# Kernel tuning notes

Hardware: AMD Instinct MI355X
Metric: run time of the kernel (lower is better)

The kernel has to match this reference:

```python
import jax, jax.numpy as jnp
import numpy as np

N = 100000      # nodes
E = 1250000     # edges
F_IN = 32       # node_feat_dim
H = 64          # hidden_dim (hard-coded in module)
R = 8           # num_relations
G = 256         # graphs in batch
EMB = 16        # embedding_dim
OUT = 1         # output_dim
EPS = 1e-5


def setup_inputs() -> dict:
    key = jax.random.key(0)
    ks = jax.random.split(key, 40)
    w = lambda k, shape: (jax.random.normal(k, shape, jnp.float32) * 0.05)
    inp = {
        'x': jax.random.normal(ks[0], (N, F_IN), jnp.float32),
        'edge_index': jax.random.randint(ks[1], (2, E), 0, N),
        'edge_type': jax.random.randint(ks[2], (E,), 0, R),
        'batch': jnp.sort(jax.random.randint(ks[3], (N,), 0, G)),
        # RGCN layer params: per-relation weight, root weight, bias
        'conv1_w': w(ks[4], (R, F_IN, H)), 'conv1_root': w(ks[5], (F_IN, H)), 'conv1_b': jnp.zeros((H,), jnp.float32),
        'bn1_g': jnp.ones((H,), jnp.float32), 'bn1_b': jnp.zeros((H,), jnp.float32),
        'conv2_w': w(ks[6], (R, H, H)), 'conv2_root': w(ks[7], (H, H)), 'conv2_b': jnp.zeros((H,), jnp.float32),
        'bn2_g': jnp.ones((H,), jnp.float32), 'bn2_b': jnp.zeros((H,), jnp.float32),
        'conv3_w': w(ks[8], (R, H, H)), 'conv3_root': w(ks[9], (H, H)), 'conv3_b': jnp.zeros((H,), jnp.float32),
        'bn3_g': jnp.ones((H,), jnp.float32), 'bn3_b': jnp.zeros((H,), jnp.float32),
        # fc_emb: Linear(384->128), BN(128), LeakyReLU, Dropout(eval=id), Linear(128->EMB)
        'fc1_w': w(ks[10], (3 * H * 2, 128)), 'fc1_b': jnp.zeros((128,), jnp.float32),
        'fcbn_g': jnp.ones((128,), jnp.float32), 'fcbn_b': jnp.zeros((128,), jnp.float32),
        'fc2_w': w(ks[11], (128, EMB)), 'fc2_b': jnp.zeros((EMB,), jnp.float32),
        # decoder: Linear(EMB->64), LeakyReLU, Linear(64->OUT)
        'dec1_w': w(ks[12], (EMB, 64)), 'dec1_b': jnp.zeros((64,), jnp.float32),
        'dec2_w': w(ks[13], (64, OUT)), 'dec2_b': jnp.zeros((OUT,), jnp.float32),
    }
    return inp


def _leaky(z):
    return jnp.where(z > 0, z, 0.2 * z)


def _bn(x, g, b):  # training-mode batch norm, biased variance
    mu = x.mean(axis=0)
    var = x.var(axis=0)
    return g * (x - mu) * jax.lax.rsqrt(var + EPS) + b


def _rgcn(x, W, root, bias, src, dst, edge_type):
    # out_i = x_i @ root + bias + sum_r mean_{j in N_r(i)} x_j @ W_r
    out = x @ root + bias
    for r in range(R):
        mask = (edge_type == r).astype(x.dtype)           # [E]
        h = x @ W[r]                                      # [N, out]
        msg = h[src] * mask[:, None]                      # gather + mask
        s = jax.ops.segment_sum(msg, dst, num_segments=N)  # scatter-add
        cnt = jax.ops.segment_sum(mask, dst, num_segments=N)
        out = out + s / jnp.maximum(cnt, 1.0)[:, None]
    return out


def reference(x, edge_index, edge_type, batch,
              conv1_w, conv1_root, conv1_b, bn1_g, bn1_b,
              conv2_w, conv2_root, conv2_b, bn2_g, bn2_b,
              conv3_w, conv3_root, conv3_b, bn3_g, bn3_b,
              fc1_w, fc1_b, fcbn_g, fcbn_b, fc2_w, fc2_b,
              dec1_w, dec1_b, dec2_w, dec2_b):
    src, dst = edge_index[0], edge_index[1]
    x1 = jax.nn.relu(_bn(_rgcn(x, conv1_w, conv1_root, conv1_b, src, dst, edge_type), bn1_g, bn1_b))
    x2 = jax.nn.relu(_bn(_rgcn(x1, conv2_w, conv2_root, conv2_b, src, dst, edge_type), bn2_g, bn2_b))
    x3 = jax.nn.relu(_bn(_rgcn(x2, conv3_w, conv3_root, conv3_b, src, dst, edge_type), bn3_g, bn3_b))
    x_all = jnp.concatenate([x1, x2, x3], axis=1)         # [N, 3H]
    ones = jnp.ones((N,), x.dtype)
    cnt = jax.ops.segment_sum(ones, batch, num_segments=G)
    pool_mean = jax.ops.segment_sum(x_all, batch, num_segments=G) / jnp.maximum(cnt, 1.0)[:, None]
    pool_max = jax.ops.segment_max(x_all, batch, num_segments=G)
    pool_max = jnp.where(jnp.isfinite(pool_max), pool_max, 0.0)
    x_graph = jnp.concatenate([pool_mean, pool_max], axis=1)  # [G, 6H]
    h = _leaky(_bn(x_graph @ fc1_w + fc1_b, fcbn_g, fcbn_b))  # dropout = identity (eval)
    emb = h @ fc2_w + fc2_b                                   # [G, EMB]
    pred = _leaky(emb @ dec1_w + dec1_b) @ dec2_w + dec2_b    # [G, OUT]
    return (pred, emb)
```

## Files before the change

### kernel.cpp

```cpp
#include <hip/hip_runtime.h>

#define NN 100000
#define NE 1250000
#define FIN 32
#define HD 64
#define NR 8
#define NG 256
#define BN_EPS 1e-5f
#define PCH 100
#define M_KEYS (NN * NR)
#define NB 782
#define RREP 32
#define HW 576

#if defined(__has_builtin)
#if __has_builtin(__builtin_amdgcn_fdot2_f32_bf16)
#define USE_DOT2 1
#endif
#endif
#ifndef USE_DOT2
#define USE_DOT2 0
#endif

typedef unsigned short ushort_t;
typedef __attribute__((ext_vector_type(8))) short short8;
typedef __attribute__((ext_vector_type(4))) float f32x4;
typedef __attribute__((ext_vector_type(4))) unsigned int u32x4;
#if USE_DOT2
typedef __bf16 bf16x2 __attribute__((ext_vector_type(2)));
#endif

static __device__ __forceinline__ ushort_t f2bf(float f) {
  unsigned u = __float_as_uint(f);
  u += 0x7fffu + ((u >> 16) & 1u);
  return (ushort_t)(u >> 16);
}
static __device__ __forceinline__ float bf2f(ushort_t b) {
  return __uint_as_float((unsigned)b << 16);
}

__global__ void k_zero(float* __restrict__ p, int n) {
  int i = blockIdx.x * 256 + threadIdx.x;
  if (i < n) p[i] = 0.0f;
}

__global__ void k_cnt(const int* __restrict__ dst, const int* __restrict__ ty,
                      unsigned* __restrict__ cnt, int* __restrict__ rank) {
  int e = blockIdx.x * 256 + threadIdx.x;
  if (e < NE) {
    int key = dst[e] * NR + ty[e];
    rank[e] = (int)atomicAdd(&cnt[key], 1u);
  }
}

__global__ void k_scanA(const unsigned* __restrict__ cnt, unsigned* __restrict__ bsum) {
  __shared__ unsigned red[256];
  int t = threadIdx.x;
  int base = blockIdx.x * 1024 + t * 4;
  unsigned s = 0;
  #pragma unroll
  for (int i = 0; i < 4; i++) {
    int idx = base + i;
    if (idx < M_KEYS) s += cnt[idx];
  }
  red[t] = s;
  __syncthreads();
  for (int off = 128; off > 0; off >>= 1) {
    if (t < off) red[t] += red[t + off];
    __syncthreads();
  }
  if (t == 0) bsum[blockIdx.x] = red[0];
}

__global__ __launch_bounds__(1024) void k_scanB(const unsigned* __restrict__ bsum,
                                                unsigned* __restrict__ boff,
                                                int* __restrict__ rowstart) {
  __shared__ unsigned sb[1024];
  int t = threadIdx.x;
  unsigned mine = (t < NB) ? bsum[t] : 0u;
  sb[t] = mine;
  __syncthreads();
  for (int off = 1; off < 1024; off <<= 1) {
    unsigned v = (t >= off) ? sb[t - off] : 0u;
    __syncthreads();
    sb[t] += v;
    __syncthreads();
  }
  if (t < NB) boff[t] = sb[t] - mine;
  if (t == 1023) rowstart[M_KEYS] = (int)sb[1023];
}

__global__ void k_scanC(const unsigned* __restrict__ cnt, const unsigned* __restrict__ boff,
                        int* __restrict__ rowstart) {
  __shared__ unsigned sb[256];
  int t = threadIdx.x;
  int base = blockIdx.x * 1024 + t * 4;
  unsigned c0 = (base + 0 < M_KEYS) ? cnt[base + 0] : 0u;
  unsigned c1 = (base + 1 < M_KEYS) ? cnt[base + 1] : 0u;
  unsigned c2 = (base + 2 < M_KEYS) ? cnt[base + 2] : 0u;
  unsigned c3 = (base + 3 < M_KEYS) ? cnt[base + 3] : 0u;
  unsigned tot = c0 + c1 + c2 + c3;
  sb[t] = tot;
  __syncthreads();
  for (int off = 1; off < 256; off <<= 1) {
    unsigned v = (t >= off) ? sb[t - off] : 0u;
    __syncthreads();
    sb[t] += v;
    __syncthreads();
  }
  unsigned run = boff[blockIdx.x] + (sb[t] - tot);
  if (base + 0 < M_KEYS) rowstart[base + 0] = (int)run; run += c0;
  if (base + 1 < M_KEYS) rowstart[base + 1] = (int)run; run += c1;
  if (base + 2 < M_KEYS) rowstart[base + 2] = (int)run; run += c2;
  if (base + 3 < M_KEYS) rowstart[base + 3] = (int)run;
}

__global__ void k_place(const int* __restrict__ src, const int* __restrict__ dst,
                        const int* __restrict__ ty, const int* __restrict__ rank,
                        const int* __restrict__ rowstart, unsigned* __restrict__ eb) {
  int e = blockIdx.x * 256 + threadIdx.x;
  if (e < NE) {
    int t = ty[e];
    int key = dst[e] * NR + t;
    unsigned off = (unsigned)(src[e] * HW + t * 64);
    eb[rowstart[key] + rank[e]] = (off << 3) | (unsigned)t;
  }
}

template <int F>
__global__ void k_wconv(const float* __restrict__ convw, const float* __restrict__ root,
                        ushort_t* __restrict__ wt) {
  int i = blockIdx.x * 256 + threadIdx.x;
  if (i >= 576 * F) return;
  int c = i / F, k = i % F;
  float v = (c < 512) ? convw[((size_t)(c >> 6) * F + k) * 64 + (c & 63)]
                      : root[(size_t)k * 64 + (c & 63)];
  wt[(size_t)c * F + k] = f2bf(v);
}

template <int F, bool APPLY_BN>
__global__ __launch_bounds__(256) void k_xmm(
    const float* __restrict__ xin, const float* __restrict__ scsh,
    const ushort_t* __restrict__ wt, ushort_t* __restrict__ h) {
  constexpr int KK = 2 * F;
  constexpr int XPAD = KK + 8;
  constexpr int LDR = 592;
  __shared__ ushort_t xs[16 * XPAD];
  __shared__ ushort_t ot[16 * LDR];
  int lane = threadIdx.x & 63;
  int w = threadIdx.x >> 6;
  int m = lane & 15;
  int q = lane >> 4;
  int ct0 = w * 9;

  short8 bfrag[9 * (F / 32)];
  #pragma unroll
  for (int ks = 0; ks < F / 32; ks++)
    #pragma unroll
    for (int t = 0; t < 9; t++)
      bfrag[ks * 9 + t] =
          *(const short8*)(wt + (size_t)((ct0 + t) * 16 + m) * F + ks * 32 + q * 8);

  for (int tile = blockIdx.x; tile < NN / 16; tile += gridDim.x) {
    int nbase = tile * 16;
    for (int i = threadIdx.x; i < 16 * F; i += 256) {
      int r = i / F, k = i - r * F;
      float v = xin[(size_t)(nbase + r) * F + k];
      if (APPLY_BN) v = fmaxf(fmaf(v, scsh[k], scsh[64 + k]), 0.0f);
      ushort_t hi = f2bf(v);
      xs[r * XPAD + k] = hi;
      xs[r * XPAD + F + k] = f2bf(v - bf2f(hi));
    }
    __syncthreads();

    short8 afrag[2 * (F / 32)];
    #pragma unroll
    for (int ks = 0; ks < F / 32; ks++) {
      afrag[2 * ks + 0] = *(const short8*)&xs[m * XPAD + ks * 32 + q * 8];
      afrag[2 * ks + 1] = *(const short8*)&xs[m * XPAD + F + ks * 32 + q * 8];
    }

    f32x4 acc[9];
    #pragma unroll
    for (int t = 0; t < 9; t++) acc[t] = (f32x4){0.f, 0.f, 0.f, 0.f};
    #pragma unroll
    for (int ks = 0; ks < F / 32; ks++) {
      #pragma unroll
      for (int t = 0; t < 9; t++) {
        acc[t] = __builtin_amdgcn_mfma_f32_16x16x32_bf16(afrag[2 * ks + 0],
                                                         bfrag[ks * 9 + t], acc[t], 0, 0, 0);
        acc[t] = __builtin_amdgcn_mfma_f32_16x16x32_bf16(afrag[2 * ks + 1],
                                                         bfrag[ks * 9 + t], acc[t], 0, 0, 0);
      }
    }
    #pragma unroll
    for (int t = 0; t < 9; t++) {
      int col = (ct0 + t) * 16 + m;
      #pragma unroll
      for (int j = 0; j < 4; j++) {
        int row = q * 4 + j;
        ot[row * LDR + col] = f2bf(acc[t][j]);
      }
    }
    __syncthreads();
    u32x4* dst = (u32x4*)(h + (size_t)nbase * HW);
    for (int idx = threadIdx.x; idx < 16 * 72; idx += 256) {
      int row = idx / 72, i = idx - row * 72;
      dst[row * 72 + i] = *(const u32x4*)&ot[row * LDR + i * 8];
    }
  }
}

__global__ __launch_bounds__(256) void k_agg4(
    const ushort_t* __restrict__ h, const int* __restrict__ rs,
    const unsigned* __restrict__ eb, const float* __restrict__ bias,
    float* __restrict__ outp, float* __restrict__ statsrep) {
  __shared__ float red[512];
  __shared__ ushort_t iclu[4][8];
  int lane = threadIdx.x & 63, w = threadIdx.x >> 6;
  int n = blockIdx.x * 4 + w;
  if (lane < 8) {
    int c = rs[n * NR + lane + 1] - rs[n * NR + lane];
    iclu[w][lane] = f2bf(1.0f / (float)(c > 1 ? c : 1));
  }
  int lo = rs[n * NR];
  int cnt = rs[n * NR + NR] - lo;
  __syncthreads();
  int g = lane >> 3;
  int c8 = (lane & 7) * 8;
  float a[8];
  #pragma unroll
  for (int j = 0; j < 8; j++) a[j] = 0.f;
  for (int base = 0; base < cnt; base += 32) {
    unsigned rec[4]; u32x4 hv[4]; unsigned icb[4];
    #pragma unroll
    for (int s = 0; s < 4; s++) {
      int el = base + s * 8 + g;
      rec[s] = eb[lo + (el < cnt ? el : cnt - 1)];
      icb[s] = (el < cnt) ? (unsigned)iclu[w][rec[s] & 7] : 0u;
    }
    #pragma unroll
    for (int s = 0; s < 4; s++)
      hv[s] = *(const u32x4*)(h + (size_t)(rec[s] >> 3) + c8);
#if USE_DOT2
    #pragma unroll
    for (int s = 0; s < 4; s += 2) {
      unsigned b01 = __builtin_amdgcn_perm(icb[s + 1], icb[s], 0x05040100u);
      bf16x2 bb = __builtin_bit_cast(bf16x2, b01);
      #pragma unroll
      for (int k = 0; k < 4; k++) {
        unsigned plo = __builtin_amdgcn_perm(hv[s + 1][k], hv[s][k], 0x05040100u);
        unsigned phi = __builtin_amdgcn_perm(hv[s + 1][k], hv[s][k], 0x07060302u);
        a[2 * k + 0] = __builtin_amdgcn_fdot2_f32_bf16(
            __builtin_bit_cast(bf16x2, plo), bb, a[2 * k + 0], false);
        a[2 * k + 1] = __builtin_amdgcn_fdot2_f32_bf16(
            __builtin_bit_cast(bf16x2, phi), bb, a[2 * k + 1], false);
      }
    }
#else
    #pragma unroll
    for (int s = 0; s < 4; s++) {
      float ic = bf2f((ushort_t)icb[s]);
      #pragma unroll
      for (int k = 0; k < 4; k++) {
        a[2 * k + 0] = fmaf(__uint_as_float(hv[s][k] << 16), ic, a[2 * k + 0]);
        a[2 * k + 1] = fmaf(__uint_as_float(hv[s][k] & 0xffff0000u), ic, a[2 * k + 1]);
      }
    }
#endif
  }
  #pragma unroll
  for (int j = 0; j < 8; j++) {
    a[j] += __shfl_xor(a[j], 8);
    a[j] += __shfl_xor(a[j], 16);
    a[j] += __shfl_xor(a[j], 32);
  }
  if (g == 0) {
    u32x4 sv = *(const u32x4*)(h + (size_t)n * HW + 512 + c8);
    float d[8];
    #pragma unroll
    for (int k = 0; k < 4; k++) {
      d[2 * k + 0] = a[2 * k + 0] + __uint_as_float(sv[k] << 16) + bias[c8 + 2 * k + 0];
      d[2 * k + 1] = a[2 * k + 1] + __uint_as_float(sv[k] & 0xffff0000u) + bias[c8 + 2 * k + 1];
    }
    float4 lo4 = make_float4(d[0], d[1], d[2], d[3]);
    float4 hi4 = make_float4(d[4], d[5], d[6], d[7]);
    *(float4*)(outp + (size_t)n * HD + c8) = lo4;
    *(float4*)(outp + (size_t)n * HD + c8 + 4) = hi4;
    *(float4*)(&red[w * 64 + c8]) = lo4;
    *(float4*)(&red[w * 64 + c8 + 4]) = hi4;
    *(float4*)(&red[256 + w * 64 + c8]) =
        make_float4(d[0] * d[0], d[1] * d[1], d[2] * d[2], d[3] * d[3]);
    *(float4*)(&red[256 + w * 64 + c8 + 4]) =
        make_float4(d[4] * d[4], d[5] * d[5], d[6] * d[6], d[7] * d[7]);
  }
  __syncthreads();
  if (w == 0) {
    float ts = red[lane] + red[64 + lane] + red[128 + lane] + red[192 + lane];
    float tss = red[256 + lane] + red[320 + lane] + red[384 + lane] + red[448 + lane];
    int rp = blockIdx.x & (RREP - 1);
    atomicAdd(&statsrep[rp * 128 + lane], ts);
    atomicAdd(&statsrep[rp * 128 + 64 + lane], tss);
  }
}

__global__ void k_finstats(const float* __restrict__ rep, const float* __restrict__ g,
                           const float* __restrict__ b, float* __restrict__ scsh) {
  int lane = threadIdx.x;
  float s = 0.f, ss = 0.f;
  for (int rp = 0; rp < RREP; rp++) {
    s += rep[rp * 128 + lane];
    ss += rep[rp * 128 + 64 + lane];
  }
  float mu = s * (1.0f / NN);
  float var = ss * (1.0f / NN) - mu * mu;
  float sc = g[lane] * rsqrtf(var + BN_EPS);
  scsh[lane] = sc;
  scsh[64 + lane] = b[lane] - mu * sc;
}

__global__ void k_poolseg(const float* __restrict__ t1, const float* __restrict__ t2,
                          const float* __restrict__ t3, const float* __restrict__ scsh,
                          const int* __restrict__ batch, float* __restrict__ psum,
                          unsigned* __restrict__ pmax, float* __restrict__ cntg) {
  __shared__ int bsh[PCH];
  int base = blockIdx.x * PCH;
  int c = threadIdx.x;
  for (int i = c; i < PCH; i += 192) bsh[i] = batch[base + i];
  __syncthreads();
  int L = c >> 6, cc = c & 63;
  const float* xs = (L == 0) ? t1 : (L == 1) ? t2 : t3;
  float sc = scsh[L * 128 + cc], sh = scsh[L * 128 + 64 + cc];
  int cur = bsh[0];
  float sum = 0.0f, mx = 0.0f;
  int runlen = 0;
  #pragma unroll 4
  for (int i = 0; i < PCH; i++) {
    int g = bsh[i];
    float v = fmaxf(fmaf(xs[(size_t)(base + i) * 64 + cc], sc, sh), 0.0f);
    if (g != cur) {
      atomicAdd(&psum[cur * 192 + c], sum);
      atomicMax(&pmax[cur * 192 + c], __float_as_uint(mx));
      if (c == 0) atomicAdd(&cntg[cur], (float)runlen);
      cur = g; sum = 0.0f; mx = 0.0f; runlen = 0;
    }
    sum += v;
    mx = fmaxf(mx, v);
    runlen++;
  }
  atomicAdd(&psum[cur * 192 + c], sum);
  atomicMax(&pmax[cur * 192 + c], __float_as_uint(mx));
  if (c == 0) atomicAdd(&cntg[cur], (float)runlen);
}

__global__ void k_fc1(const float* __restrict__ psum, const unsigned* __restrict__ pmax,
                      const float* __restrict__ cntg, const float* __restrict__ w,
                      const float* __restrict__ bias, float* __restrict__ h1) {
  __shared__ float a[384];
  int g = blockIdx.x;
  float ic = 1.0f / fmaxf(cntg[g], 1.0f);
  for (int c = threadIdx.x; c < 384; c += 128) {
    a[c] = (c < 192) ? psum[g * 192 + c] * ic : __uint_as_float(pmax[g * 192 + (c - 192)]);
  }
  __syncthreads();
  int j = threadIdx.x;
  float acc = bias[j];
  for (int k = 0; k < 384; k++) acc = fmaf(a[k], w[k * 128 + j], acc);
  h1[g * 128 + j] = acc;
}

__global__ void k_fcbn_stats(const float* __restrict__ h1, const float* __restrict__ g,
                             const float* __restrict__ b, float* __restrict__ scsh) {
  __shared__ float sr[512], ssr[512];
  int j = threadIdx.x & 127, q = threadIdx.x >> 7;
  float s = 0.f, ss = 0.f;
  for (int i = q * 64; i < q * 64 + 64; i++) {
    float v = h1[i * 128 + j];
    s += v;
    ss = fmaf(v, v, ss);
  }
  sr[threadIdx.x] = s;
  ssr[threadIdx.x] = ss;
  __syncthreads();
  if (q == 0) {
    s = sr[j] + sr[128 + j] + sr[256 + j] + sr[384 + j];
    ss = ssr[j] + ssr[128 + j] + ssr[256 + j] + ssr[384 + j];
    float mu = s * (1.0f / NG);
    float var = ss * (1.0f / NG) - mu * mu;
    float sc = g[j] * rsqrtf(var + BN_EPS);
    scsh[j] = sc;
    scsh[128 + j] = b[j] - mu * sc;
  }
}

__global__ void k_leaky(float* __restrict__ h1, const float* __restrict__ scsh) {
  int j = threadIdx.x;
  int g = blockIdx.x;
  float v = fmaf(h1[g * 128 + j], scsh[j], scsh[128 + j]);
  h1[g * 128 + j] = v > 0.0f ? v : 0.2f * v;
}

__global__ void k_head(const float* __restrict__ h1, const float* __restrict__ fc2w,
                       const float* __restrict__ fc2b, const float* __restrict__ d1w,
                       const float* __restrict__ d1b, const float* __restrict__ d2w,
                       const float* __restrict__ d2b, float* __restrict__ out) {
  __shared__ float emb[16];
  int g = blockIdx.x;
  int t = threadIdx.x;
  if (t < 16) {
    float acc = fc2b[t];
    for (int k = 0; k < 128; k++) acc = fmaf(h1[g * 128 + k], fc2w[k * 16 + t], acc);
    emb[t] = acc;
    out[NG + g * 16 + t] = acc;
  }
  __syncthreads();
  float acc = d1b[t];
  for (int k = 0; k < 16; k++) acc = fmaf(emb[k], d1w[k * 64 + t], acc);
  acc = acc > 0.0f ? acc : 0.2f * acc;
  float p = acc * d2w[t];
  for (int off = 32; off > 0; off >>= 1) p += __shfl_down(p, off);
  if (t == 0) out[g] = p + d2b[0];
}

extern "C" void kernel_launch(void* const* d_in, const int* in_sizes, int n_in,
                              void* d_out, int out_size, void* d_ws, size_t ws_size,
                              hipStream_t stream) {
  const float* x    = (const float*)d_in[0];
  const int*   ei   = (const int*)d_in[1];
  const int*   ety  = (const int*)d_in[2];
  const int*   batch= (const int*)d_in[3];
  const float* c1w  = (const float*)d_in[4];
  const float* c1r  = (const float*)d_in[5];
  const float* c1b  = (const float*)d_in[6];
  const float* bn1g = (const float*)d_in[7];
  const float* bn1b = (const float*)d_in[8];
  const float* c2w  = (const float*)d_in[9];
  const float* c2r  = (const float*)d_in[10];
  const float* c2b  = (const float*)d_in[11];
  const float* bn2g = (const float*)d_in[12];
  const float* bn2b = (const float*)d_in[13];
  const float* c3w  = (const float*)d_in[14];
  const float* c3r  = (const float*)d_in[15];
  const float* c3b  = (const float*)d_in[16];
  const float* bn3g = (const float*)d_in[17];
  const float* bn3b = (const float*)d_in[18];
  const float* fc1w = (const float*)d_in[19];
  const float* fc1b = (const float*)d_in[20];
  const float* fbg  = (const float*)d_in[21];
  const float* fbb  = (const float*)d_in[22];
  const float* fc2w = (const float*)d_in[23];
  const float* fc2b = (const float*)d_in[24];
  const float* d1w  = (const float*)d_in[25];
  const float* d1b  = (const float*)d_in[26];
  const float* d2w  = (const float*)d_in[27];
  const float* d2b  = (const float*)d_in[28];
  const int* esrc = ei;
  const int* edst = ei + NE;
  float* out = (float*)d_out;

  float* W = (float*)d_ws;
  size_t o = 0;
  auto alloc = [&](size_t n) { float* p = W + o; o += (n + 63) & ~(size_t)63; return p; };
  unsigned* cnt      = (unsigned*)alloc(M_KEYS);
  float*    psum     = alloc(NG * 192);
  unsigned* pmax     = (unsigned*)alloc(NG * 192);
  float*    cntg     = alloc(NG);
  float*    statsrep = alloc(3 * RREP * 128);
  size_t zone = o;
  int*      rowstart = (int*)alloc(M_KEYS + 1);
  int*      rank = (int*)alloc(NE);
  unsigned* eb   = (unsigned*)alloc(NE);
  unsigned* bsum = (unsigned*)alloc(1024);
  unsigned* boff = (unsigned*)alloc(1024);
  float*    scsh = alloc(3 * 128);
  float*    fcsc = alloc(256);
  float*    h1   = alloc(NG * 128);
  float*    tmp1 = alloc((size_t)NN * HD);
  float*    tmp2 = alloc((size_t)NN * HD);
  float*    tmp3 = alloc((size_t)NN * HD);
  ushort_t* hbig = (ushort_t*)alloc((size_t)NN * HW / 2);
  ushort_t* wt1  = (ushort_t*)alloc(576 * FIN / 2);
  ushort_t* wt2  = (ushort_t*)alloc(576 * HD / 2);
  ushort_t* wt3  = (ushort_t*)alloc(576 * HD / 2);
  (void)ws_size; (void)in_sizes; (void)n_in; (void)out_size;

  k_zero<<<(int)((zone + 255) / 256), 256, 0, stream>>>(W, (int)zone);
  k_cnt<<<(NE + 255) / 256, 256, 0, stream>>>(edst, ety, cnt, rank);
  k_scanA<<<NB, 256, 0, stream>>>(cnt, bsum);
  k_scanB<<<1, 1024, 0, stream>>>(bsum, boff, rowstart);
  k_scanC<<<NB, 256, 0, stream>>>(cnt, boff, rowstart);
  k_place<<<(NE + 255) / 256, 256, 0, stream>>>(esrc, edst, ety, rank, rowstart, eb);
  k_wconv<FIN><<<(576 * FIN + 255) / 256, 256, 0, stream>>>(c1w, c1r, wt1);
  k_wconv<HD><<<(576 * HD + 255) / 256, 256, 0, stream>>>(c2w, c2r, wt2);
  k_wconv<HD><<<(576 * HD + 255) / 256, 256, 0, stream>>>(c3w, c3r, wt3);

  k_xmm<FIN, false><<<2048, 256, 0, stream>>>(x, nullptr, wt1, hbig);
  k_agg4<<<NN / 4, 256, 0, stream>>>(hbig, rowstart, eb, c1b, tmp1, statsrep);
  k_finstats<<<1, 64, 0, stream>>>(statsrep, bn1g, bn1b, scsh);

  k_xmm<HD, true><<<2048, 256, 0, stream>>>(tmp1, scsh, wt2, hbig);
  k_agg4<<<NN / 4, 256, 0, stream>>>(hbig, rowstart, eb, c2b, tmp2, statsrep + RREP * 128);
  k_finstats<<<1, 64, 0, stream>>>(statsrep + RREP * 128, bn2g, bn2b, scsh + 128);

  k_xmm<HD, true><<<2048, 256, 0, stream>>>(tmp2, scsh + 128, wt3, hbig);
  k_agg4<<<NN / 4, 256, 0, stream>>>(hbig, rowstart, eb, c3b, tmp3, statsrep + 2 * RREP * 128);
  k_finstats<<<1, 64, 0, stream>>>(statsrep + 2 * RREP * 128, bn3g, bn3b, scsh + 256);

  k_poolseg<<<NN / PCH, 192, 0, stream>>>(tmp1, tmp2, tmp3, scsh, batch, psum, pmax, cntg);
  k_fc1<<<NG, 128, 0, stream>>>(psum, pmax, cntg, fc1w, fc1b, h1);
  k_fcbn_stats<<<1, 512, 0, stream>>>(h1, fbg, fbb, fcsc);
  k_leaky<<<NG, 128, 0, stream>>>(h1, fcsc);
  k_head<<<NG, 64, 0, stream>>>(h1, fc2w, fc2b, d1w, d1b, d2w, d2b, out);
}
```

Baseline: 447.0 us.

## Build per-node CSR instead of per-(node,relation) and half-wave aggregation per node

The edge sort now produces a CSR keyed by destination node only. Counts are still kept per (node, relation) to compute the mean normalisation, but the scan runs over nodes, which shrinks the scan arrays and removes the rank array. Placement uses an atomic cursor per node instead of precomputed ranks. Aggregation now assigns a half-wavefront to each node, so each block covers 8 nodes, which improves utilisation for low-degree nodes. The cost is a non-deterministic edge order within each node and some wasted work when the two nodes sharing a wave have different degrees.

After: 460.0 us. 1.03x slower.

```diff
diff --git a/kernel.cpp b/kernel.cpp
--- a/kernel.cpp
+++ b/kernel.cpp
@@ -9,7 +9,7 @@
 #define BN_EPS 1e-5f
 #define PCH 100
 #define M_KEYS (NN * NR)
-#define NB 782
+#define NBN 98
 #define RREP 32
 #define HW 576
 
@@ -45,23 +45,24 @@
 }
 
 __global__ void k_cnt(const int* __restrict__ dst, const int* __restrict__ ty,
-                      unsigned* __restrict__ cnt, int* __restrict__ rank) {
+                      unsigned* __restrict__ cnt8) {
   int e = blockIdx.x * 256 + threadIdx.x;
-  if (e < NE) {
-    int key = dst[e] * NR + ty[e];
-    rank[e] = (int)atomicAdd(&cnt[key], 1u);
-  }
-}
-
-__global__ void k_scanA(const unsigned* __restrict__ cnt, unsigned* __restrict__ bsum) {
+  if (e < NE) atomicAdd(&cnt8[dst[e] * NR + ty[e]], 1u);
+}
+
+__global__ void k_scanA(const unsigned* __restrict__ cnt8, unsigned* __restrict__ bsum) {
   __shared__ unsigned red[256];
   int t = threadIdx.x;
   int base = blockIdx.x * 1024 + t * 4;
   unsigned s = 0;
   #pragma unroll
   for (int i = 0; i < 4; i++) {
-    int idx = base + i;
-    if (idx < M_KEYS) s += cnt[idx];
+    int nd = base + i;
+    if (nd < NN) {
+      const u32x4* p = (const u32x4*)(cnt8 + (size_t)nd * NR);
+      u32x4 v0 = p[0], v1 = p[1];
+      s += v0[0] + v0[1] + v0[2] + v0[3] + v1[0] + v1[1] + v1[2] + v1[3];
+    }
   }
   red[t] = s;
   __syncthreads();
@@ -77,7 +78,7 @@
                                                 int* __restrict__ rowstart) {
   __shared__ unsigned sb[1024];
   int t = threadIdx.x;
-  unsigned mine = (t < NB) ? bsum[t] : 0u;
+  unsigned mine = (t < NBN) ? bsum[t] : 0u;
   sb[t] = mine;
   __syncthreads();
   for (int off = 1; off < 1024; off <<= 1) {
@@ -86,20 +87,29 @@
     sb[t] += v;
     __syncthreads();
   }
-  if (t < NB) boff[t] = sb[t] - mine;
-  if (t == 1023) rowstart[M_KEYS] = (int)sb[1023];
-}
-
-__global__ void k_scanC(const unsigned* __restrict__ cnt, const unsigned* __restrict__ boff,
-                        int* __restrict__ rowstart) {
+  if (t < NBN) boff[t] = sb[t] - mine;
+  if (t == 1023) rowstart[NN] = (int)sb[1023];
+}
+
+__global__ void k_scanC(const unsigned* __restrict__ cnt8, const unsigned* __restrict__ boff,
+                        int* __restrict__ rowstart, int* __restrict__ pos) {
   __shared__ unsigned sb[256];
   int t = threadIdx.x;
   int base = blockIdx.x * 1024 + t * 4;
-  unsigned c0 = (base + 0 < M_KEYS) ? cnt[base + 0] : 0u;
-  unsigned c1 = (base + 1 < M_KEYS) ? cnt[base + 1] : 0u;
-  unsigned c2 = (base + 2 < M_KEYS) ? cnt[base + 2] : 0u;
-  unsigned c3 = (base + 3 < M_KEYS) ? cnt[base + 3] : 0u;
-  unsigned tot = c0 + c1 + c2 + c3;
+  unsigned d[4];
+  unsigned tot = 0;
+  #pragma unroll
+  for (int i = 0; i < 4; i++) {
+    unsigned s = 0;
+    int nd = base + i;
+    if (nd < NN) {
+      const u32x4* p = (const u32x4*)(cnt8 + (size_t)nd * NR);
+      u32x4 v0 = p[0], v1 = p[1];
+      s = v0[0] + v0[1] + v0[2] + v0[3] + v1[0] + v1[1] + v1[2] + v1[3];
+    }
+    d[i] = s;
+    tot += s;
+  }
   sb[t] = tot;
   __syncthreads();
   for (int off = 1; off < 256; off <<= 1) {
@@ -109,21 +119,24 @@
     __syncthreads();
   }
   unsigned run = boff[blockIdx.x] + (sb[t] - tot);
-  if (base + 0 < M_KEYS) rowstart[base + 0] = (int)run; run += c0;
-  if (base + 1 < M_KEYS) rowstart[base + 1] = (int)run; run += c1;
-  if (base + 2 < M_KEYS) rowstart[base + 2] = (int)run; run += c2;
-  if (base + 3 < M_KEYS) rowstart[base + 3] = (int)run;
+  #pragma unroll
+  for (int i = 0; i < 4; i++) {
+    int nd = base + i;
+    if (nd < NN) { rowstart[nd] = (int)run; pos[nd] = (int)run; }
+    run += d[i];
+  }
 }
 
 __global__ void k_place(const int* __restrict__ src, const int* __restrict__ dst,
-                        const int* __restrict__ ty, const int* __restrict__ rank,
-                        const int* __restrict__ rowstart, unsigned* __restrict__ eb) {
+                        const int* __restrict__ ty, int* __restrict__ pos,
+                        unsigned* __restrict__ eb) {
   int e = blockIdx.x * 256 + threadIdx.x;
   if (e < NE) {
     int t = ty[e];
-    int key = dst[e] * NR + t;
+    int d = dst[e];
     unsigned off = (unsigned)(src[e] * HW + t * 64);
-    eb[rowstart[key] + rank[e]] = (off << 3) | (unsigned)t;
+    int p = atomicAdd(&pos[d], 1);
+    eb[p] = (off << 3) | (unsigned)t;
   }
 }
 
@@ -212,32 +225,38 @@
 }
 
 __global__ __launch_bounds__(256) void k_agg4(
-    const ushort_t* __restrict__ h, const int* __restrict__ rs,
-    const unsigned* __restrict__ eb, const float* __restrict__ bias,
-    float* __restrict__ outp, float* __restrict__ statsrep) {
-  __shared__ float red[512];
-  __shared__ ushort_t iclu[4][8];
+    const ushort_t* __restrict__ h, const int* __restrict__ rowstart,
+    const unsigned* __restrict__ cnt8, const unsigned* __restrict__ eb,
+    const float* __restrict__ bias, float* __restrict__ outp,
+    float* __restrict__ statsrep) {
+  __shared__ float red[1024];
+  __shared__ ushort_t iclu[8][8];
   int lane = threadIdx.x & 63, w = threadIdx.x >> 6;
-  int n = blockIdx.x * 4 + w;
-  if (lane < 8) {
-    int c = rs[n * NR + lane + 1] - rs[n * NR + lane];
-    iclu[w][lane] = f2bf(1.0f / (float)(c > 1 ? c : 1));
-  }
-  int lo = rs[n * NR];
-  int cnt = rs[n * NR + NR] - lo;
-  __syncthreads();
-  int g = lane >> 3;
+  int hw = lane >> 5;
+  int nd = w * 2 + hw;
+  int n = blockIdx.x * 8 + nd;
+  int l32 = lane & 31;
+  if (l32 < 8) {
+    unsigned c = cnt8[(size_t)n * NR + l32];
+    iclu[nd][l32] = f2bf(1.0f / (float)(c > 1u ? c : 1u));
+  }
+  int lo = rowstart[n];
+  int cnt = rowstart[n + 1] - lo;
+  __syncthreads();
+  int g = (lane >> 3) & 3;
   int c8 = (lane & 7) * 8;
+  int cntmax = max(cnt, __shfl_xor(cnt, 32));
   float a[8];
   #pragma unroll
   for (int j = 0; j < 8; j++) a[j] = 0.f;
-  for (int base = 0; base < cnt; base += 32) {
+  for (int base = 0; base < cntmax; base += 16) {
     unsigned rec[4]; u32x4 hv[4]; unsigned icb[4];
     #pragma unroll
     for (int s = 0; s < 4; s++) {
-      int el = base + s * 8 + g;
-      rec[s] = eb[lo + (el < cnt ? el : cnt - 1)];
-      icb[s] = (el < cnt) ? (unsigned)iclu[w][rec[s] & 7] : 0u;
+      int el = base + s * 4 + g;
+      int ee = (el < cnt) ? el : (cnt > 0 ? cnt - 1 : 0);
+      rec[s] = eb[lo + ee];
+      icb[s] = (el < cnt) ? (unsigned)iclu[nd][rec[s] & 7] : 0u;
     }
     #pragma unroll
     for (int s = 0; s < 4; s++)
@@ -273,31 +292,39 @@
   for (int j = 0; j < 8; j++) {
     a[j] += __shfl_xor(a[j], 8);
     a[j] += __shfl_xor(a[j], 16);
-    a[j] += __shfl_xor(a[j], 32);
   }
   if (g == 0) {
     u32x4 sv = *(const u32x4*)(h + (size_t)n * HW + 512 + c8);
+    float4 b4lo = *(const float4*)(bias + c8);
+    float4 b4hi = *(const float4*)(bias + c8 + 4);
     float d[8];
-    #pragma unroll
-    for (int k = 0; k < 4; k++) {
-      d[2 * k + 0] = a[2 * k + 0] + __uint_as_float(sv[k] << 16) + bias[c8 + 2 * k + 0];
-      d[2 * k + 1] = a[2 * k + 1] + __uint_as_float(sv[k] & 0xffff0000u) + bias[c8 + 2 * k + 1];
-    }
+    d[0] = a[0] + __uint_as_float(sv[0] << 16) + b4lo.x;
+    d[1] = a[1] + __uint_as_float(sv[0] & 0xffff0000u) + b4lo.y;
+    d[2] = a[2] + __uint_as_float(sv[1] << 16) + b4lo.z;
+    d[3] = a[3] + __uint_as_float(sv[1] & 0xffff0000u) + b4lo.w;
+    d[4] = a[4] + __uint_as_float(sv[2] << 16) + b4hi.x;
+    d[5] = a[5] + __uint_as_float(sv[2] & 0xffff0000u) + b4hi.y;
+    d[6] = a[6] + __uint_as_float(sv[3] << 16) + b4hi.z;
+    d[7] = a[7] + __uint_as_float(sv[3] & 0xffff0000u) + b4hi.w;
     float4 lo4 = make_float4(d[0], d[1], d[2], d[3]);
     float4 hi4 = make_float4(d[4], d[5], d[6], d[7]);
     *(float4*)(outp + (size_t)n * HD + c8) = lo4;
     *(float4*)(outp + (size_t)n * HD + c8 + 4) = hi4;
-    *(float4*)(&red[w * 64 + c8]) = lo4;
-    *(float4*)(&red[w * 64 + c8 + 4]) = hi4;
-    *(float4*)(&red[256 + w * 64 + c8]) =
+    *(float4*)(&red[nd * 64 + c8]) = lo4;
+    *(float4*)(&red[nd * 64 + c8 + 4]) = hi4;
+    *(float4*)(&red[512 + nd * 64 + c8]) =
         make_float4(d[0] * d[0], d[1] * d[1], d[2] * d[2], d[3] * d[3]);
-    *(float4*)(&red[256 + w * 64 + c8 + 4]) =
+    *(float4*)(&red[512 + nd * 64 + c8 + 4]) =
         make_float4(d[4] * d[4], d[5] * d[5], d[6] * d[6], d[7] * d[7]);
   }
   __syncthreads();
   if (w == 0) {
-    float ts = red[lane] + red[64 + lane] + red[128 + lane] + red[192 + lane];
-    float tss = red[256 + lane] + red[320 + lane] + red[384 + lane] + red[448 + lane];
+    float ts = 0.f, tss = 0.f;
+    #pragma unroll
+    for (int k = 0; k < 8; k++) {
+      ts += red[k * 64 + lane];
+      tss += red[512 + k * 64 + lane];
+    }
     int rp = blockIdx.x & (RREP - 1);
     atomicAdd(&statsrep[rp * 128 + lane], ts);
     atomicAdd(&statsrep[rp * 128 + 64 + lane], tss);
@@ -461,14 +488,14 @@
   float* W = (float*)d_ws;
   size_t o = 0;
   auto alloc = [&](size_t n) { float* p = W + o; o += (n + 63) & ~(size_t)63; return p; };
-  unsigned* cnt      = (unsigned*)alloc(M_KEYS);
+  unsigned* cnt8     = (unsigned*)alloc(M_KEYS);
   float*    psum     = alloc(NG * 192);
   unsigned* pmax     = (unsigned*)alloc(NG * 192);
   float*    cntg     = alloc(NG);
   float*    statsrep = alloc(3 * RREP * 128);
   size_t zone = o;
-  int*      rowstart = (int*)alloc(M_KEYS + 1);
-  int*      rank = (int*)alloc(NE);
+  int*      rowstart = (int*)alloc(NN + 1);
+  int*      pos  = (int*)alloc(NN + 1);
   unsigned* eb   = (unsigned*)alloc(NE);
   unsigned* bsum = (unsigned*)alloc(1024);
   unsigned* boff = (unsigned*)alloc(1024);
@@ -485,25 +512,25 @@
   (void)ws_size; (void)in_sizes; (void)n_in; (void)out_size;
 
   k_zero<<<(int)((zone + 255) / 256), 256, 0, stream>>>(W, (int)zone);
-  k_cnt<<<(NE + 255) / 256, 256, 0, stream>>>(edst, ety, cnt, rank);
-  k_scanA<<<NB, 256, 0, stream>>>(cnt, bsum);
+  k_cnt<<<(NE + 255) / 256, 256, 0, stream>>>(edst, ety, cnt8);
+  k_scanA<<<NBN, 256, 0, stream>>>(cnt8, bsum);
   k_scanB<<<1, 1024, 0, stream>>>(bsum, boff, rowstart);
-  k_scanC<<<NB, 256, 0, stream>>>(cnt, boff, rowstart);
-  k_place<<<(NE + 255) / 256, 256, 0, stream>>>(esrc, edst, ety, rank, rowstart, eb);
+  k_scanC<<<NBN, 256, 0, stream>>>(cnt8, boff, rowstart, pos);
+  k_place<<<(NE + 255) / 256, 256, 0, stream>>>(esrc, edst, ety, pos, eb);
   k_wconv<FIN><<<(576 * FIN + 255) / 256, 256, 0, stream>>>(c1w, c1r, wt1);
   k_wconv<HD><<<(576 * HD + 255) / 256, 256, 0, stream>>>(c2w, c2r, wt2);
   k_wconv<HD><<<(576 * HD + 255) / 256, 256, 0, stream>>>(c3w, c3r, wt3);
 
   k_xmm<FIN, false><<<2048, 256, 0, stream>>>(x, nullptr, wt1, hbig);
-  k_agg4<<<NN / 4, 256, 0, stream>>>(hbig, rowstart, eb, c1b, tmp1, statsrep);
+  k_agg4<<<NN / 8, 256, 0, stream>>>(hbig, rowstart, cnt8, eb, c1b, tmp1, statsrep);
   k_finstats<<<1, 64, 0, stream>>>(statsrep, bn1g, bn1b, scsh);
 
   k_xmm<HD, true><<<2048, 256, 0, stream>>>(tmp1, scsh, wt2, hbig);
-  k_agg4<<<NN / 4, 256, 0, stream>>>(hbig, rowstart, eb, c2b, tmp2, statsrep + RREP * 128);
+  k_agg4<<<NN / 8, 256, 0, stream>>>(hbig, rowstart, cnt8, eb, c2b, tmp2, statsrep + RREP * 128);
   k_finstats<<<1, 64, 0, stream>>>(statsrep + RREP * 128, bn2g, bn2b, scsh + 128);
 
   k_xmm<HD, true><<<2048, 256, 0, stream>>>(tmp2, scsh + 128, wt3, hbig);
-  k_agg4<<<NN / 4, 256, 0, stream>>>(hbig, rowstart, eb, c3b, tmp3, statsrep + 2 * RREP * 128);
+  k_agg4<<<NN / 8, 256, 0, stream>>>(hbig, rowstart, cnt8, eb, c3b, tmp3, statsrep + 2 * RREP * 128);
   k_finstats<<<1, 64, 0, stream>>>(statsrep + 2 * RREP * 128, bn3g, bn3b, scsh + 256);
 
   k_poolseg<<<NN / PCH, 192, 0, stream>>>(tmp1, tmp2, tmp3, scsh, batch, psum, pmax, cntg);
```
